# Kernel tuning notes

Measured on AMD Instinct MI355X. Metric: run time of the kernel, lower is better.

Reference implementation:

```python
import jax, jax.numpy as jnp
import numpy as np

B, S, E, H = 4, 1024, 1024, 16
HD = E // H


def setup_inputs() -> dict:
    key = jax.random.key(0)
    k1, k2, k3 = jax.random.split(key, 3)
    hidden_states = jax.random.normal(k1, (B, S, E), dtype=jnp.float32)
    attention_mask = jnp.ones((B, S), dtype=jnp.int32)
    STD = 0.02
    W_qkv = jax.random.normal(k2, (E, 3 * E), dtype=jnp.float32) * STD
    b_qkv = jnp.zeros((3 * E,), dtype=jnp.float32)
    W_proj = jax.random.normal(k3, (E, E), dtype=jnp.float32) * STD
    b_proj = jnp.zeros((E,), dtype=jnp.float32)
    return {
        "hidden_states": hidden_states,
        "attention_mask": attention_mask,
        "W_qkv": W_qkv,
        "b_qkv": b_qkv,
        "W_proj": W_proj,
        "b_proj": b_proj,
    }


def reference(hidden_states, attention_mask, W_qkv, b_qkv, W_proj, b_proj):
    b, s, _ = hidden_states.shape
    dtype = hidden_states.dtype
    qkv = hidden_states @ W_qkv + b_qkv  # [b, s, 3E]
    q, k, v = jnp.split(qkv, 3, axis=-1)

    def split_heads(x):
        return x.reshape(b, s, H, HD).transpose(0, 2, 1, 3)  # [b, H, s, hd]

    q, k, v = split_heads(q), split_heads(k), split_heads(v)
    scale = jnp.asarray(HD, dtype=dtype) ** (-0.5)
    scores = jnp.einsum("bnth,bnsh->bnts", q, k) * scale  # [b, H, s, s]
    causal = jnp.tril(jnp.ones((s, s), dtype=bool))
    key_mask = attention_mask.astype(bool)  # [b, s]
    full_mask = causal[None, None, :, :] & key_mask[:, None, None, :]
    neg = jnp.asarray(jnp.finfo(dtype).min, dtype=dtype)
    bias = jnp.where(full_mask, jnp.asarray(0.0, dtype=dtype), neg)
    probs = jax.nn.softmax(scores + bias, axis=-1)
    out = jnp.einsum("bnts,bnsh->bnth", probs, v)  # [b, H, s, hd]
    out = out.transpose(0, 2, 1, 3).reshape(b, s, E)
    return out @ W_proj + b_proj
```

## Files before the change

### kernel.cpp

```cpp
#include <hip/hip_runtime.h>
#include <stdint.h>

typedef __attribute__((ext_vector_type(8))) short bf16x8;
typedef __attribute__((ext_vector_type(4))) float f32x4;
typedef unsigned short u16;

__device__ __forceinline__ float bf2f(u16 b) {
    unsigned int u = ((unsigned int)b) << 16;
    return __builtin_bit_cast(float, u);
}
__device__ __forceinline__ u16 f2bf(float f) {
    unsigned int u = __builtin_bit_cast(unsigned int, f);
    u += 0x7fffu + ((u >> 16) & 1u);
    return (u16)(u >> 16);
}
__device__ __forceinline__ u16 f2bf_trunc(float f) {
    return (u16)(__builtin_bit_cast(unsigned int, f) >> 16);
}

__device__ __forceinline__ void gl2lds16(const u16* g, u16* l) {
    __builtin_amdgcn_global_load_lds(
        (const __attribute__((address_space(1))) unsigned int*)g,
        (__attribute__((address_space(3))) unsigned int*)l, 16, 0, 0);
}

__global__ __launch_bounds__(256) void cvt_kernel(const float* __restrict__ in,
                                                  u16* __restrict__ out, long n) {
    long i = ((long)blockIdx.x * 256 + threadIdx.x) * 4;
    if (i >= n) return;
    float4 v = *(const float4*)(in + i);
    alignas(8) u16 o[4] = {f2bf(v.x), f2bf(v.y), f2bf(v.z), f2bf(v.w)};
    *(uint2*)(out + i) = *(const uint2*)o;
}

__global__ __launch_bounds__(256) void cvt_transpose(const float* __restrict__ in,
                                                     u16* __restrict__ out, int R, int C) {
    __shared__ float t[64][68];
    int c0 = blockIdx.x * 64, r0 = blockIdx.y * 64, tid = threadIdx.x;
#pragma unroll
    for (int i = 0; i < 4; i++) {
        int ch = i * 256 + tid;
        int r = ch >> 4, cc = (ch & 15) * 4;
        float4 v = *(const float4*)(in + (long)(r0 + r) * C + c0 + cc);
        *(float4*)&t[r][cc] = v;
    }
    __syncthreads();
#pragma unroll
    for (int i = 0; i < 2; i++) {
        int ch = i * 256 + tid;
        int cw = ch >> 3, rr = (ch & 7) * 8;
        alignas(16) u16 tmp[8];
#pragma unroll
        for (int j = 0; j < 8; j++) tmp[j] = f2bf(t[rr + j][cw]);
        *(int4*)(out + (long)(c0 + cw) * R + r0 + rr) = *(const int4*)tmp;
    }
}

__global__ __launch_bounds__(256) void build_vt(const u16* __restrict__ v_tmp,
                                                const int* __restrict__ amask,
                                                u16* __restrict__ vt) {
    __shared__ u16 t[64][72];
    __shared__ u16 mv[64];
    int bh = blockIdx.y, b = bh >> 4, s0 = blockIdx.x * 64, tid = threadIdx.x;
    const u16* inb = v_tmp + ((long)bh * 1024 + s0) * 64;
#pragma unroll
    for (int i = 0; i < 2; i++) {
        int ch = i * 256 + tid;
        int r = ch >> 3, c = (ch & 7) * 8;
        *(int4*)&t[r][c] = *(const int4*)(inb + r * 64 + c);
    }
    if (tid < 64) mv[tid] = amask[b * 1024 + s0 + tid] ? 1 : 0;
    __syncthreads();
    u16* outb = vt + (long)bh * 80 * 1024 + s0;
#pragma unroll
    for (int i = 0; i < 3; i++) {
        int ch = i * 256 + tid;
        if (ch < 640) {
            int row = ch >> 3, c8 = (ch & 7) * 8;
            alignas(16) u16 tmp[8];
#pragma unroll
            for (int jj = 0; jj < 8; jj++) {
                int key = c8 + jj;
                u16 val = (row < 64) ? t[key][row] : ((row == 64) ? (u16)0x3F80 : (u16)0);
                tmp[jj] = mv[key] ? val : (u16)0;
            }
            *(int4*)(outb + (long)row * 1024 + c8) = *(const int4*)tmp;
        }
    }
}

__global__ __launch_bounds__(256) void gemm_bt(
    const u16* __restrict__ X, const u16* __restrict__ Wt,
    const float* __restrict__ bias,
    u16* __restrict__ o0, u16* __restrict__ o1, u16* __restrict__ o2,
    float* __restrict__ outF,
    int M, int N, int K, int mode) {
    __shared__ u16 As[128 * 32];
    __shared__ u16 Bs[128 * 32];
    const int tid = threadIdx.x;
    const int m0 = blockIdx.y * 128, n0 = blockIdx.x * 128;
    const int w = tid >> 6, lane = tid & 63, l16 = lane & 15, quad = lane >> 4;
    const int wm = (w >> 1) * 64, wn = (w & 1) * 64;

    f32x4 acc[4][4];
    const f32x4 z = {0.f, 0.f, 0.f, 0.f};
#pragma unroll
    for (int i = 0; i < 4; i++)
#pragma unroll
        for (int j = 0; j < 4; j++) acc[i][j] = z;

    for (int k0 = 0; k0 < K; k0 += 32) {
        if (k0) __syncthreads();
#pragma unroll
        for (int i = 0; i < 2; i++) {
            int slot = i * 256 + tid;
            int row = slot >> 2, gp = slot & 3;
            int g = gp ^ ((row >> 1) & 3);
            gl2lds16(X + (long)(m0 + row) * K + k0 + g * 8, &As[slot * 8]);
            gl2lds16(Wt + (long)(n0 + row) * K + k0 + g * 8, &Bs[slot * 8]);
        }
        __syncthreads();
        bf16x8 af[4], bfr[4];
#pragma unroll
        for (int mt = 0; mt < 4; mt++) {
            int row = wm + mt * 16 + l16;
            int g = quad ^ ((row >> 1) & 3);
            af[mt] = *(const bf16x8*)&As[row * 32 + g * 8];
        }
#pragma unroll
        for (int nt = 0; nt < 4; nt++) {
            int row = wn + nt * 16 + l16;
            int g = quad ^ ((row >> 1) & 3);
            bfr[nt] = *(const bf16x8*)&Bs[row * 32 + g * 8];
        }
#pragma unroll
        for (int mt = 0; mt < 4; mt++)
#pragma unroll
            for (int nt = 0; nt < 4; nt++)
                acc[mt][nt] = __builtin_amdgcn_mfma_f32_16x16x32_bf16(
                    af[mt], bfr[nt], acc[mt][nt], 0, 0, 0);
    }

#pragma unroll
    for (int nt = 0; nt < 4; nt++) {
        int n = n0 + wn + nt * 16 + l16;
        float bias_v = bias[n];
#pragma unroll
        for (int mt = 0; mt < 4; mt++) {
#pragma unroll
            for (int r = 0; r < 4; r++) {
                int m = m0 + wm + mt * 16 + quad * 4 + r;
                float val = acc[mt][nt][r] + bias_v;
                if (mode == 0) {
                    outF[(long)m * N + n] = val;
                } else {
                    int which = n >> 10, e = n & 1023, h = e >> 6, d = e & 63;
                    int b = m >> 10, s = m & 1023;
                    long adr = ((long)(b * 16 + h) * 1024 + s) * 64 + d;
                    u16* dst = (which == 0) ? o0 : (which == 1) ? o1 : o2;
                    dst[adr] = f2bf(val);
                }
            }
        }
    }
}

#define PPAD 88
__global__ __launch_bounds__(256) void attn_kernel(
    const u16* __restrict__ Q, const u16* __restrict__ K,
    const u16* __restrict__ Vt, u16* __restrict__ O) {
    const int S = 1024;
    const int idx = blockIdx.x;
    const int qb = 15 - (idx >> 6);
    const int bh = idx & 63, b = bh >> 4, h = bh & 15;
    const int tid = threadIdx.x, w = tid >> 6, lane = tid & 63;
    const int l16 = lane & 15, quad = lane >> 4;
    const int q0 = qb * 64 + w * 16;

    __shared__ u16 kt[2][64 * 64];
    __shared__ u16 vt[2][80 * 64];
    __shared__ u16 p_lds[4][16][PPAD];

    const u16* Qb = Q + (long)bh * S * 64;
    const u16* Kb = K + (long)bh * S * 64;
    const u16* Vb = Vt + (long)bh * 80 * S;

    const float C = 0.125f * 1.4426950408889634f;
    bf16x8 qf[2];
#pragma unroll
    for (int kc = 0; kc < 2; kc++) {
        bf16x8 qr = *(const bf16x8*)(Qb + (q0 + l16) * 64 + kc * 32 + quad * 8);
        bf16x8 qs;
#pragma unroll
        for (int e = 0; e < 8; e++) qs[e] = (short)f2bf(bf2f((u16)qr[e]) * C);
        qf[kc] = qs;
    }

    const f32x4 z = {0.f, 0.f, 0.f, 0.f};
    f32x4 o_acc[5];
#pragma unroll
    for (int nt = 0; nt < 5; nt++) o_acc[nt] = z;

    auto prefetch = [&](int j, int pb) {
#pragma unroll
        for (int i = 0; i < 2; i++) {
            int slot = i * 256 + tid;
            int row = slot >> 3, gp = slot & 7;
            int g = gp ^ (row & 7);
            gl2lds16(Kb + (j * 64 + row) * 64 + g * 8, &kt[pb][slot * 8]);
        }
#pragma unroll
        for (int i = 0; i < 3; i++) {
            int slot = i * 256 + tid;
            if (slot < 640) {
                int row = slot >> 3, gp = slot & 7;
                int g = gp ^ (row & 7);
                gl2lds16(Vb + (long)row * S + j * 64 + g * 8, &vt[pb][slot * 8]);
            }
        }
    };

    prefetch(0, 0);
    for (int j = 0; j <= qb; j++) {
        int buf = j & 1;
        __syncthreads();
        if (j < qb) prefetch(j + 1, buf ^ 1);

        f32x4 s_acc[4];
#pragma unroll
        for (int nt = 0; nt < 4; nt++) s_acc[nt] = z;
#pragma unroll
        for (int nt = 0; nt < 4; nt++) {
            int row = nt * 16 + l16;
#pragma unroll
            for (int kc = 0; kc < 2; kc++) {
                int g = (kc * 4 + quad) ^ (row & 7);
                bf16x8 kf = *(const bf16x8*)&kt[buf][row * 64 + g * 8];
                s_acc[nt] = __builtin_amdgcn_mfma_f32_16x16x32_bf16(qf[kc], kf, s_acc[nt], 0, 0, 0);
            }
        }
        float p[4][4];
#pragma unroll
        for (int nt = 0; nt < 4; nt++)
#pragma unroll
            for (int r = 0; r < 4; r++) p[nt][r] = exp2f(s_acc[nt][r]);
        if (j == qb) {
#pragma unroll
            for (int nt = 0; nt < 4; nt++) {
                int key = j * 64 + nt * 16 + l16;
#pragma unroll
                for (int r = 0; r < 4; r++)
                    if (key > q0 + quad * 4 + r) p[nt][r] = 0.f;
            }
        }
#pragma unroll
        for (int nt = 0; nt < 4; nt++)
#pragma unroll
            for (int r = 0; r < 4; r++)
                p_lds[w][quad * 4 + r][nt * 16 + l16] = f2bf_trunc(p[nt][r]);
        bf16x8 pf[2];
#pragma unroll
        for (int kc = 0; kc < 2; kc++)
            pf[kc] = *(const bf16x8*)&p_lds[w][l16][kc * 32 + quad * 8];
#pragma unroll
        for (int nt = 0; nt < 5; nt++) {
            int row = nt * 16 + l16;
#pragma unroll
            for (int kc = 0; kc < 2; kc++) {
                int g = (kc * 4 + quad) ^ (row & 7);
                bf16x8 vf = *(const bf16x8*)&vt[buf][row * 64 + g * 8];
                o_acc[nt] = __builtin_amdgcn_mfma_f32_16x16x32_bf16(pf[kc], vf, o_acc[nt], 0, 0, 0);
            }
        }
    }
#pragma unroll
    for (int r = 0; r < 4; r++) {
        float l = __shfl(o_acc[4][r], lane & 48, 64);
        float inv = 1.0f / l;
        int qg = q0 + quad * 4 + r;
#pragma unroll
        for (int nt = 0; nt < 4; nt++)
            O[((long)(b * S + qg)) * 1024 + h * 64 + nt * 16 + l16] = f2bf(o_acc[nt][r] * inv);
    }
}

extern "C" void kernel_launch(void* const* d_in, const int* in_sizes, int n_in,
                              void* d_out, int out_size, void* d_ws, size_t ws_size,
                              hipStream_t stream) {
    const float* hs    = (const float*)d_in[0];
    const int*   amask = (const int*)d_in[1];
    const float* Wqkv  = (const float*)d_in[2];
    const float* bqkv  = (const float*)d_in[3];
    const float* Wproj = (const float*)d_in[4];
    const float* bproj = (const float*)d_in[5];
    float* out = (float*)d_out;

    const long ME = 4096L * 1024L;
    size_t need = (3072L * 1024 + ME + 1024L * 1024 + 3 * ME) * 2;
    if (ws_size < need) return;

    u16* wqkv_t  = (u16*)d_ws;
    u16* hs_bf   = wqkv_t + 3072L * 1024;
    u16* wproj_t = hs_bf + ME;
    u16* q_ws    = wproj_t + 1024L * 1024;
    u16* k_ws    = q_ws + ME;
    u16* v_tmp   = k_ws + ME;
    u16* vt_aug  = (u16*)d_ws;
    u16* attn_out= v_tmp;

    dim3 blk(256);
    cvt_kernel<<<dim3(4096), blk, 0, stream>>>(hs, hs_bf, ME);
    cvt_transpose<<<dim3(48, 16), blk, 0, stream>>>(Wqkv, wqkv_t, 1024, 3072);
    cvt_transpose<<<dim3(16, 16), blk, 0, stream>>>(Wproj, wproj_t, 1024, 1024);
    gemm_bt<<<dim3(24, 32), blk, 0, stream>>>(hs_bf, wqkv_t, bqkv, q_ws, k_ws, v_tmp,
                                              nullptr, 4096, 3072, 1024, 1);
    build_vt<<<dim3(16, 64), blk, 0, stream>>>(v_tmp, amask, vt_aug);
    attn_kernel<<<dim3(1024), blk, 0, stream>>>(q_ws, k_ws, vt_aug, attn_out);
    gemm_bt<<<dim3(8, 32), blk, 0, stream>>>(attn_out, wproj_t, bproj, nullptr, nullptr, nullptr,
                                             out, 4096, 1024, 1024, 0);
}
```

Measured before the change: 181.9 us.

## Stage QKV GEMM epilogue through LDS and double attention query tile

The QKV GEMM epilogue now converts results to bf16 and stages them in shared memory in two halves, then writes 16-byte vectors to the head-split Q/K/V buffers. Before, each thread wrote scattered 2-byte stores. The attention kernel now handles 128 query rows per block, 32 per wave, so each K/V tile loaded into LDS serves twice as many queries, and the grid is halved to 512 blocks. The costs are an extra 16KB of LDS and more registers in the GEMM, fewer and longer attention blocks with more load imbalance from the causal mask, and waves that sit idle on tiles above their diagonal.

Measured after the change: 201.0 us. 10.5% more time.

```diff
diff --git a/kernel.cpp b/kernel.cpp
--- a/kernel.cpp
+++ b/kernel.cpp
@@ -97,6 +97,7 @@
     int M, int N, int K, int mode) {
     __shared__ u16 As[128 * 32];
     __shared__ u16 Bs[128 * 32];
+    __shared__ u16 ostage[64 * 128];
     const int tid = threadIdx.x;
     const int m0 = blockIdx.y * 128, n0 = blockIdx.x * 128;
     const int w = tid >> 6, lane = tid & 63, l16 = lane & 15, quad = lane >> 4;
@@ -141,65 +142,96 @@
                     af[mt], bfr[nt], acc[mt][nt], 0, 0, 0);
     }
 
-#pragma unroll
-    for (int nt = 0; nt < 4; nt++) {
-        int n = n0 + wn + nt * 16 + l16;
-        float bias_v = bias[n];
-#pragma unroll
-        for (int mt = 0; mt < 4; mt++) {
-#pragma unroll
-            for (int r = 0; r < 4; r++) {
-                int m = m0 + wm + mt * 16 + quad * 4 + r;
-                float val = acc[mt][nt][r] + bias_v;
-                if (mode == 0) {
-                    outF[(long)m * N + n] = val;
-                } else {
-                    int which = n >> 10, e = n & 1023, h = e >> 6, d = e & 63;
-                    int b = m >> 10, s = m & 1023;
-                    long adr = ((long)(b * 16 + h) * 1024 + s) * 64 + d;
-                    u16* dst = (which == 0) ? o0 : (which == 1) ? o1 : o2;
-                    dst[adr] = f2bf(val);
+    if (mode == 0) {
+#pragma unroll
+        for (int nt = 0; nt < 4; nt++) {
+            int n = n0 + wn + nt * 16 + l16;
+            float bias_v = bias[n];
+#pragma unroll
+            for (int mt = 0; mt < 4; mt++)
+#pragma unroll
+                for (int r = 0; r < 4; r++) {
+                    int m = m0 + wm + mt * 16 + quad * 4 + r;
+                    outF[(long)m * N + n] = acc[mt][nt][r] + bias_v;
                 }
-            }
-        }
-    }
-}
-
-#define PPAD 88
+        }
+    } else {
+#pragma unroll
+        for (int p = 0; p < 2; p++) {
+            if (p) __syncthreads();
+            if ((w >> 1) == p) {
+#pragma unroll
+                for (int nt = 0; nt < 4; nt++) {
+                    int col = wn + nt * 16 + l16;
+                    float bias_v = bias[n0 + col];
+#pragma unroll
+                    for (int mt = 0; mt < 4; mt++)
+#pragma unroll
+                        for (int r = 0; r < 4; r++) {
+                            int row = mt * 16 + quad * 4 + r;
+                            int gs = (col >> 3) ^ ((row >> 1) & 7);
+                            ostage[row * 128 + gs * 8 + (col & 7)] =
+                                f2bf(acc[mt][nt][r] + bias_v);
+                        }
+                }
+            }
+            __syncthreads();
+#pragma unroll
+            for (int i = 0; i < 4; i++) {
+                int g = i * 256 + tid;
+                int rr = g >> 4, c = (g >> 3) & 1, seg = g & 7;
+                int gs = (c * 8 + seg) ^ ((rr >> 1) & 7);
+                int4 v = *(const int4*)&ostage[rr * 128 + gs * 8];
+                int m = m0 + p * 64 + rr;
+                int nbase = n0 + c * 64;
+                int which = nbase >> 10, e = nbase & 1023, hh = e >> 6;
+                int bb = m >> 10, s = m & 1023;
+                u16* dst = (which == 0) ? o0 : (which == 1) ? o1 : o2;
+                *(int4*)(dst + (((long)(bb * 16 + hh) * 1024 + s) * 64 + seg * 8)) = v;
+            }
+        }
+    }
+}
+
+#define QPAD 76
 __global__ __launch_bounds__(256) void attn_kernel(
     const u16* __restrict__ Q, const u16* __restrict__ K,
     const u16* __restrict__ Vt, u16* __restrict__ O) {
     const int S = 1024;
     const int idx = blockIdx.x;
-    const int qb = 15 - (idx >> 6);
+    const int qb = 7 - (idx >> 6);
     const int bh = idx & 63, b = bh >> 4, h = bh & 15;
     const int tid = threadIdx.x, w = tid >> 6, lane = tid & 63;
     const int l16 = lane & 15, quad = lane >> 4;
-    const int q0 = qb * 64 + w * 16;
+    const int q0 = qb * 128 + w * 32;
 
     __shared__ u16 kt[2][64 * 64];
     __shared__ u16 vt[2][80 * 64];
-    __shared__ u16 p_lds[4][16][PPAD];
+    __shared__ u16 p_lds[4][32][QPAD];
 
     const u16* Qb = Q + (long)bh * S * 64;
     const u16* Kb = K + (long)bh * S * 64;
     const u16* Vb = Vt + (long)bh * 80 * S;
 
     const float C = 0.125f * 1.4426950408889634f;
-    bf16x8 qf[2];
-#pragma unroll
-    for (int kc = 0; kc < 2; kc++) {
-        bf16x8 qr = *(const bf16x8*)(Qb + (q0 + l16) * 64 + kc * 32 + quad * 8);
-        bf16x8 qs;
-#pragma unroll
-        for (int e = 0; e < 8; e++) qs[e] = (short)f2bf(bf2f((u16)qr[e]) * C);
-        qf[kc] = qs;
-    }
+    bf16x8 qf[2][2];
+#pragma unroll
+    for (int qt = 0; qt < 2; qt++)
+#pragma unroll
+        for (int kc = 0; kc < 2; kc++) {
+            bf16x8 qr = *(const bf16x8*)(Qb + (q0 + qt * 16 + l16) * 64 + kc * 32 + quad * 8);
+            bf16x8 qs;
+#pragma unroll
+            for (int e = 0; e < 8; e++) qs[e] = (short)f2bf(bf2f((u16)qr[e]) * C);
+            qf[qt][kc] = qs;
+        }
 
     const f32x4 z = {0.f, 0.f, 0.f, 0.f};
-    f32x4 o_acc[5];
-#pragma unroll
-    for (int nt = 0; nt < 5; nt++) o_acc[nt] = z;
+    f32x4 o_acc[2][5];
+#pragma unroll
+    for (int qt = 0; qt < 2; qt++)
+#pragma unroll
+        for (int nt = 0; nt < 5; nt++) o_acc[qt][nt] = z;
 
     auto prefetch = [&](int j, int pb) {
 #pragma unroll
@@ -221,67 +253,90 @@
     };
 
     prefetch(0, 0);
-    for (int j = 0; j <= qb; j++) {
+    const int jmax = 2 * qb + 1;
+    for (int j = 0; j <= jmax; j++) {
         int buf = j & 1;
         __syncthreads();
-        if (j < qb) prefetch(j + 1, buf ^ 1);
-
-        f32x4 s_acc[4];
-#pragma unroll
-        for (int nt = 0; nt < 4; nt++) s_acc[nt] = z;
-#pragma unroll
-        for (int nt = 0; nt < 4; nt++) {
-            int row = nt * 16 + l16;
-#pragma unroll
-            for (int kc = 0; kc < 2; kc++) {
-                int g = (kc * 4 + quad) ^ (row & 7);
-                bf16x8 kf = *(const bf16x8*)&kt[buf][row * 64 + g * 8];
-                s_acc[nt] = __builtin_amdgcn_mfma_f32_16x16x32_bf16(qf[kc], kf, s_acc[nt], 0, 0, 0);
-            }
-        }
-        float p[4][4];
-#pragma unroll
-        for (int nt = 0; nt < 4; nt++)
-#pragma unroll
-            for (int r = 0; r < 4; r++) p[nt][r] = exp2f(s_acc[nt][r]);
-        if (j == qb) {
+        if (j < jmax) prefetch(j + 1, buf ^ 1);
+
+        if (j * 64 <= q0 + 31) {
+            f32x4 s_acc[2][4];
+#pragma unroll
+            for (int qt = 0; qt < 2; qt++)
+#pragma unroll
+                for (int nt = 0; nt < 4; nt++) s_acc[qt][nt] = z;
 #pragma unroll
             for (int nt = 0; nt < 4; nt++) {
-                int key = j * 64 + nt * 16 + l16;
-#pragma unroll
-                for (int r = 0; r < 4; r++)
-                    if (key > q0 + quad * 4 + r) p[nt][r] = 0.f;
-            }
-        }
-#pragma unroll
-        for (int nt = 0; nt < 4; nt++)
-#pragma unroll
-            for (int r = 0; r < 4; r++)
-                p_lds[w][quad * 4 + r][nt * 16 + l16] = f2bf_trunc(p[nt][r]);
-        bf16x8 pf[2];
-#pragma unroll
-        for (int kc = 0; kc < 2; kc++)
-            pf[kc] = *(const bf16x8*)&p_lds[w][l16][kc * 32 + quad * 8];
-#pragma unroll
-        for (int nt = 0; nt < 5; nt++) {
-            int row = nt * 16 + l16;
-#pragma unroll
-            for (int kc = 0; kc < 2; kc++) {
-                int g = (kc * 4 + quad) ^ (row & 7);
-                bf16x8 vf = *(const bf16x8*)&vt[buf][row * 64 + g * 8];
-                o_acc[nt] = __builtin_amdgcn_mfma_f32_16x16x32_bf16(pf[kc], vf, o_acc[nt], 0, 0, 0);
-            }
-        }
-    }
-#pragma unroll
-    for (int r = 0; r < 4; r++) {
-        float l = __shfl(o_acc[4][r], lane & 48, 64);
-        float inv = 1.0f / l;
-        int qg = q0 + quad * 4 + r;
-#pragma unroll
-        for (int nt = 0; nt < 4; nt++)
-            O[((long)(b * S + qg)) * 1024 + h * 64 + nt * 16 + l16] = f2bf(o_acc[nt][r] * inv);
-    }
+                int row = nt * 16 + l16;
+#pragma unroll
+                for (int kc = 0; kc < 2; kc++) {
+                    int g = (kc * 4 + quad) ^ (row & 7);
+                    bf16x8 kf = *(const bf16x8*)&kt[buf][row * 64 + g * 8];
+#pragma unroll
+                    for (int qt = 0; qt < 2; qt++)
+                        s_acc[qt][nt] = __builtin_amdgcn_mfma_f32_16x16x32_bf16(
+                            qf[qt][kc], kf, s_acc[qt][nt], 0, 0, 0);
+                }
+            }
+            float p[2][4][4];
+#pragma unroll
+            for (int qt = 0; qt < 2; qt++)
+#pragma unroll
+                for (int nt = 0; nt < 4; nt++)
+#pragma unroll
+                    for (int r = 0; r < 4; r++) p[qt][nt][r] = exp2f(s_acc[qt][nt][r]);
+            if (j * 64 + 63 > q0) {
+#pragma unroll
+                for (int qt = 0; qt < 2; qt++)
+#pragma unroll
+                    for (int nt = 0; nt < 4; nt++) {
+                        int key = j * 64 + nt * 16 + l16;
+#pragma unroll
+                        for (int r = 0; r < 4; r++)
+                            if (key > q0 + qt * 16 + quad * 4 + r) p[qt][nt][r] = 0.f;
+                    }
+            }
+#pragma unroll
+            for (int qt = 0; qt < 2; qt++)
+#pragma unroll
+                for (int nt = 0; nt < 4; nt++)
+#pragma unroll
+                    for (int r = 0; r < 4; r++)
+                        p_lds[w][qt * 16 + quad * 4 + r][nt * 16 + l16] =
+                            f2bf_trunc(p[qt][nt][r]);
+            bf16x8 pf[2][2];
+#pragma unroll
+            for (int qt = 0; qt < 2; qt++)
+#pragma unroll
+                for (int kc = 0; kc < 2; kc++)
+                    pf[qt][kc] = *(const bf16x8*)&p_lds[w][qt * 16 + l16][kc * 32 + quad * 8];
+#pragma unroll
+            for (int vtile = 0; vtile < 5; vtile++) {
+                int row = vtile * 16 + l16;
+#pragma unroll
+                for (int kc = 0; kc < 2; kc++) {
+                    int g = (kc * 4 + quad) ^ (row & 7);
+                    bf16x8 vf = *(const bf16x8*)&vt[buf][row * 64 + g * 8];
+#pragma unroll
+                    for (int qt = 0; qt < 2; qt++)
+                        o_acc[qt][vtile] = __builtin_amdgcn_mfma_f32_16x16x32_bf16(
+                            pf[qt][kc], vf, o_acc[qt][vtile], 0, 0, 0);
+                }
+            }
+        }
+    }
+#pragma unroll
+    for (int qt = 0; qt < 2; qt++)
+#pragma unroll
+        for (int r = 0; r < 4; r++) {
+            float l = __shfl(o_acc[qt][4][r], lane & 48, 64);
+            float inv = 1.0f / l;
+            int qg = q0 + qt * 16 + quad * 4 + r;
+#pragma unroll
+            for (int nt = 0; nt < 4; nt++)
+                O[((long)(b * S + qg)) * 1024 + h * 64 + nt * 16 + l16] =
+                    f2bf(o_acc[qt][nt][r] * inv);
+        }
 }
 
 extern "C" void kernel_launch(void* const* d_in, const int* in_sizes, int n_in,
@@ -315,7 +370,7 @@
     gemm_bt<<<dim3(24, 32), blk, 0, stream>>>(hs_bf, wqkv_t, bqkv, q_ws, k_ws, v_tmp,
                                               nullptr, 4096, 3072, 1024, 1);
     build_vt<<<dim3(16, 64), blk, 0, stream>>>(v_tmp, amask, vt_aug);
-    attn_kernel<<<dim3(1024), blk, 0, stream>>>(q_ws, k_ws, vt_aug, attn_out);
+    attn_kernel<<<dim3(512), blk, 0, stream>>>(q_ws, k_ws, vt_aug, attn_out);
     gemm_bt<<<dim3(8, 32), blk, 0, stream>>>(attn_out, wproj_t, bproj, nullptr, nullptr, nullptr,
                                              out, 4096, 1024, 1024, 0);
 }
```

## Stage QKV GEMM epilogue through LDS for vectorized head-layout stores

Applied to the files above, without the earlier changes.

The GEMM warp tiling changes from a 2x2 arrangement of 64x64 tiles to four warps that each cover all 128 rows and a 32-column strip, so every warp reads all A fragments and two B fragments. In QKV mode the bf16 results are written into swizzled shared memory in two halves and then stored to the per-head Q/K/V layout as 16-byte vector writes. This replaces scattered 2-byte stores. It adds extra barriers and LDS traffic, and gives a different A/B fragment-load balance.

Result: slower. 192.5 us (+5.8%).

```diff
diff --git a/kernel.cpp b/kernel.cpp
--- a/kernel.cpp
+++ b/kernel.cpp
@@ -95,19 +95,20 @@
     u16* __restrict__ o0, u16* __restrict__ o1, u16* __restrict__ o2,
     float* __restrict__ outF,
     int M, int N, int K, int mode) {
-    __shared__ u16 As[128 * 32];
-    __shared__ u16 Bs[128 * 32];
+    __shared__ u16 smem[8192];
+    u16* As = smem;
+    u16* Bs = smem + 4096;
     const int tid = threadIdx.x;
     const int m0 = blockIdx.y * 128, n0 = blockIdx.x * 128;
     const int w = tid >> 6, lane = tid & 63, l16 = lane & 15, quad = lane >> 4;
-    const int wm = (w >> 1) * 64, wn = (w & 1) * 64;
-
-    f32x4 acc[4][4];
+    const int wn = w * 32;
+
+    f32x4 acc[8][2];
     const f32x4 z = {0.f, 0.f, 0.f, 0.f};
 #pragma unroll
-    for (int i = 0; i < 4; i++)
-#pragma unroll
-        for (int j = 0; j < 4; j++) acc[i][j] = z;
+    for (int i = 0; i < 8; i++)
+#pragma unroll
+        for (int j = 0; j < 2; j++) acc[i][j] = z;
 
     for (int k0 = 0; k0 < K; k0 += 32) {
         if (k0) __syncthreads();
@@ -120,46 +121,75 @@
             gl2lds16(Wt + (long)(n0 + row) * K + k0 + g * 8, &Bs[slot * 8]);
         }
         __syncthreads();
-        bf16x8 af[4], bfr[4];
-#pragma unroll
-        for (int mt = 0; mt < 4; mt++) {
-            int row = wm + mt * 16 + l16;
+        bf16x8 af[8], bfr[2];
+#pragma unroll
+        for (int mt = 0; mt < 8; mt++) {
+            int row = mt * 16 + l16;
             int g = quad ^ ((row >> 1) & 3);
             af[mt] = *(const bf16x8*)&As[row * 32 + g * 8];
         }
 #pragma unroll
-        for (int nt = 0; nt < 4; nt++) {
+        for (int nt = 0; nt < 2; nt++) {
             int row = wn + nt * 16 + l16;
             int g = quad ^ ((row >> 1) & 3);
             bfr[nt] = *(const bf16x8*)&Bs[row * 32 + g * 8];
         }
 #pragma unroll
-        for (int mt = 0; mt < 4; mt++)
-#pragma unroll
-            for (int nt = 0; nt < 4; nt++)
+        for (int mt = 0; mt < 8; mt++)
+#pragma unroll
+            for (int nt = 0; nt < 2; nt++)
                 acc[mt][nt] = __builtin_amdgcn_mfma_f32_16x16x32_bf16(
                     af[mt], bfr[nt], acc[mt][nt], 0, 0, 0);
     }
 
-#pragma unroll
-    for (int nt = 0; nt < 4; nt++) {
-        int n = n0 + wn + nt * 16 + l16;
-        float bias_v = bias[n];
-#pragma unroll
-        for (int mt = 0; mt < 4; mt++) {
-#pragma unroll
-            for (int r = 0; r < 4; r++) {
-                int m = m0 + wm + mt * 16 + quad * 4 + r;
-                float val = acc[mt][nt][r] + bias_v;
-                if (mode == 0) {
-                    outF[(long)m * N + n] = val;
-                } else {
-                    int which = n >> 10, e = n & 1023, h = e >> 6, d = e & 63;
-                    int b = m >> 10, s = m & 1023;
-                    long adr = ((long)(b * 16 + h) * 1024 + s) * 64 + d;
-                    u16* dst = (which == 0) ? o0 : (which == 1) ? o1 : o2;
-                    dst[adr] = f2bf(val);
+    if (mode == 0) {
+#pragma unroll
+        for (int nt = 0; nt < 2; nt++) {
+            int n = n0 + wn + nt * 16 + l16;
+            float bias_v = bias[n];
+#pragma unroll
+            for (int mt = 0; mt < 8; mt++)
+#pragma unroll
+                for (int r = 0; r < 4; r++) {
+                    int m = m0 + mt * 16 + quad * 4 + r;
+                    outF[(long)m * N + n] = acc[mt][nt][r] + bias_v;
                 }
+        }
+    } else {
+        __syncthreads();
+        u16* ostage = smem;
+#pragma unroll
+        for (int p = 0; p < 2; p++) {
+            if (p) __syncthreads();
+#pragma unroll
+            for (int mt = 0; mt < 4; mt++) {
+                int mtg = p * 4 + mt;
+#pragma unroll
+                for (int nt = 0; nt < 2; nt++) {
+                    int col = wn + nt * 16 + l16;
+                    float bias_v = bias[n0 + col];
+#pragma unroll
+                    for (int r = 0; r < 4; r++) {
+                        int row = mt * 16 + quad * 4 + r;
+                        int gs = (col >> 3) ^ ((row >> 1) & 7);
+                        ostage[row * 128 + gs * 8 + (col & 7)] =
+                            f2bf(acc[mtg][nt][r] + bias_v);
+                    }
+                }
+            }
+            __syncthreads();
+#pragma unroll
+            for (int i = 0; i < 4; i++) {
+                int g = i * 256 + tid;
+                int rr = g >> 4, c = (g >> 3) & 1, seg = g & 7;
+                int gs = (c * 8 + seg) ^ ((rr >> 1) & 7);
+                int4 v = *(const int4*)&ostage[rr * 128 + gs * 8];
+                int m = m0 + p * 64 + rr;
+                int nbase = n0 + c * 64;
+                int which = nbase >> 10, e = nbase & 1023, hh = e >> 6;
+                int bb = m >> 10, s = m & 1023;
+                u16* dst = (which == 0) ? o0 : (which == 1) ? o1 : o2;
+                *(int4*)(dst + (((long)(bb * 16 + hh) * 1024 + s) * 64 + seg * 8)) = v;
             }
         }
     }
```

## Fuse prep kernels, write masked transposed V from QKV GEMM, retile projection

Applied to the files above, without the earlier changes.

Merges the three conversion/transpose kernels into one launch. The QKV GEMM epilogue now writes V directly in transposed, masked form with a ones-row for the softmax denominator, which removes the separate build_vt pass and its round trip through memory. The attention kernel now loads only 65 V rows instead of 80 and zero-fills the padding rows in LDS once. The output projection moves to a dedicated 128x64-tile kernel with twice as many blocks. The trade-off is strided 2-byte scattered stores for transposed V in the GEMM epilogue, plus an extra mask-row load in each prefetch.

Result: faster. 174.9 us (-3.9%).

```diff
diff --git a/kernel.cpp b/kernel.cpp
--- a/kernel.cpp
+++ b/kernel.cpp
@@ -24,19 +24,31 @@
         (__attribute__((address_space(3))) unsigned int*)l, 16, 0, 0);
 }
 
-__global__ __launch_bounds__(256) void cvt_kernel(const float* __restrict__ in,
-                                                  u16* __restrict__ out, long n) {
-    long i = ((long)blockIdx.x * 256 + threadIdx.x) * 4;
-    if (i >= n) return;
-    float4 v = *(const float4*)(in + i);
-    alignas(8) u16 o[4] = {f2bf(v.x), f2bf(v.y), f2bf(v.z), f2bf(v.w)};
-    *(uint2*)(out + i) = *(const uint2*)o;
-}
-
-__global__ __launch_bounds__(256) void cvt_transpose(const float* __restrict__ in,
-                                                     u16* __restrict__ out, int R, int C) {
+__global__ __launch_bounds__(256) void prep_kernel(
+    const float* __restrict__ hs, const float* __restrict__ Wqkv,
+    const float* __restrict__ Wproj, u16* __restrict__ hs_bf,
+    u16* __restrict__ wqkv_t, u16* __restrict__ wproj_t) {
     __shared__ float t[64][68];
-    int c0 = blockIdx.x * 64, r0 = blockIdx.y * 64, tid = threadIdx.x;
+    int bx = blockIdx.x, tid = threadIdx.x;
+    if (bx < 4096) {
+        long i = ((long)bx * 256 + tid) * 4;
+        float4 v = *(const float4*)(hs + i);
+        alignas(8) u16 o[4] = {f2bf(v.x), f2bf(v.y), f2bf(v.z), f2bf(v.w)};
+        *(uint2*)(hs_bf + i) = *(const uint2*)o;
+        return;
+    }
+    const float* in;
+    u16* out;
+    int R = 1024, C, c0, r0;
+    if (bx < 4864) {
+        int tt = bx - 4096;
+        C = 3072; c0 = (tt % 48) * 64; r0 = (tt / 48) * 64;
+        in = Wqkv; out = wqkv_t;
+    } else {
+        int tt = bx - 4864;
+        C = 1024; c0 = (tt % 16) * 64; r0 = (tt / 16) * 64;
+        in = Wproj; out = wproj_t;
+    }
 #pragma unroll
     for (int i = 0; i < 4; i++) {
         int ch = i * 256 + tid;
@@ -56,45 +68,11 @@
     }
 }
 
-__global__ __launch_bounds__(256) void build_vt(const u16* __restrict__ v_tmp,
-                                                const int* __restrict__ amask,
-                                                u16* __restrict__ vt) {
-    __shared__ u16 t[64][72];
-    __shared__ u16 mv[64];
-    int bh = blockIdx.y, b = bh >> 4, s0 = blockIdx.x * 64, tid = threadIdx.x;
-    const u16* inb = v_tmp + ((long)bh * 1024 + s0) * 64;
-#pragma unroll
-    for (int i = 0; i < 2; i++) {
-        int ch = i * 256 + tid;
-        int r = ch >> 3, c = (ch & 7) * 8;
-        *(int4*)&t[r][c] = *(const int4*)(inb + r * 64 + c);
-    }
-    if (tid < 64) mv[tid] = amask[b * 1024 + s0 + tid] ? 1 : 0;
-    __syncthreads();
-    u16* outb = vt + (long)bh * 80 * 1024 + s0;
-#pragma unroll
-    for (int i = 0; i < 3; i++) {
-        int ch = i * 256 + tid;
-        if (ch < 640) {
-            int row = ch >> 3, c8 = (ch & 7) * 8;
-            alignas(16) u16 tmp[8];
-#pragma unroll
-            for (int jj = 0; jj < 8; jj++) {
-                int key = c8 + jj;
-                u16 val = (row < 64) ? t[key][row] : ((row == 64) ? (u16)0x3F80 : (u16)0);
-                tmp[jj] = mv[key] ? val : (u16)0;
-            }
-            *(int4*)(outb + (long)row * 1024 + c8) = *(const int4*)tmp;
-        }
-    }
-}
-
-__global__ __launch_bounds__(256) void gemm_bt(
+__global__ __launch_bounds__(256) void gemm_qkv(
     const u16* __restrict__ X, const u16* __restrict__ Wt,
-    const float* __restrict__ bias,
-    u16* __restrict__ o0, u16* __restrict__ o1, u16* __restrict__ o2,
-    float* __restrict__ outF,
-    int M, int N, int K, int mode) {
+    const float* __restrict__ bias, const int* __restrict__ amask,
+    u16* __restrict__ q_ws, u16* __restrict__ k_ws, u16* __restrict__ vt_ws,
+    int K) {
     __shared__ u16 As[128 * 32];
     __shared__ u16 Bs[128 * 32];
     const int tid = threadIdx.x;
@@ -141,27 +119,40 @@
                     af[mt], bfr[nt], acc[mt][nt], 0, 0, 0);
     }
 
+    const int which = n0 >> 10;
+    const int b = m0 >> 10;
+    int ncol[4]; float bv[4];
 #pragma unroll
     for (int nt = 0; nt < 4; nt++) {
-        int n = n0 + wn + nt * 16 + l16;
-        float bias_v = bias[n];
-#pragma unroll
-        for (int mt = 0; mt < 4; mt++) {
-#pragma unroll
-            for (int r = 0; r < 4; r++) {
-                int m = m0 + wm + mt * 16 + quad * 4 + r;
-                float val = acc[mt][nt][r] + bias_v;
-                if (mode == 0) {
-                    outF[(long)m * N + n] = val;
-                } else {
-                    int which = n >> 10, e = n & 1023, h = e >> 6, d = e & 63;
-                    int b = m >> 10, s = m & 1023;
-                    long adr = ((long)(b * 16 + h) * 1024 + s) * 64 + d;
-                    u16* dst = (which == 0) ? o0 : (which == 1) ? o1 : o2;
-                    dst[adr] = f2bf(val);
-                }
-            }
-        }
+        ncol[nt] = n0 + wn + nt * 16 + l16;
+        bv[nt] = bias[ncol[nt]];
+    }
+#pragma unroll
+    for (int mt = 0; mt < 4; mt++) {
+#pragma unroll
+        for (int r = 0; r < 4; r++) {
+            int m = m0 + wm + mt * 16 + quad * 4 + r;
+            int s = m & 1023;
+            float mk = 1.f;
+            if (which == 2) mk = amask[b * 1024 + s] ? 1.f : 0.f;
+#pragma unroll
+            for (int nt = 0; nt < 4; nt++) {
+                int e = ncol[nt] & 1023, h = e >> 6, d = e & 63;
+                float val = acc[mt][nt][r] + bv[nt];
+                if (which == 0)
+                    q_ws[((long)(b * 16 + h) * 1024 + s) * 64 + d] = f2bf(val);
+                else if (which == 1)
+                    k_ws[((long)(b * 16 + h) * 1024 + s) * 64 + d] = f2bf(val);
+                else
+                    vt_ws[((long)(b * 16 + h) * 65 + d) * 1024 + s] = f2bf(val * mk);
+            }
+        }
+    }
+    if (which == 2) {
+        int hh = ((n0 & 1023) >> 6) + (tid >> 7);
+        int s = (m0 & 1023) + (tid & 127);
+        vt_ws[((long)(b * 16 + hh) * 65 + 64) * 1024 + s] =
+            amask[b * 1024 + s] ? (u16)0x3F80 : (u16)0;
     }
 }
 
@@ -183,7 +174,14 @@
 
     const u16* Qb = Q + (long)bh * S * 64;
     const u16* Kb = K + (long)bh * S * 64;
-    const u16* Vb = Vt + (long)bh * 80 * S;
+    const u16* Vb = Vt + (long)bh * 65 * S;
+
+    if (tid < 240) {
+        int bufi = tid >= 120, rem = tid - bufi * 120;
+        int row = 65 + (rem >> 3), gp = rem & 7;
+        const int4 z4 = {0, 0, 0, 0};
+        *(int4*)&vt[bufi][row * 64 + gp * 8] = z4;
+    }
 
     const float C = 0.125f * 1.4426950408889634f;
     bf16x8 qf[2];
@@ -202,6 +200,9 @@
     for (int nt = 0; nt < 5; nt++) o_acc[nt] = z;
 
     auto prefetch = [&](int j, int pb) {
+        int4 mrow;
+        if (tid < 8)
+            mrow = *(const int4*)(Vb + 64 * S + j * 64 + tid * 8);
 #pragma unroll
         for (int i = 0; i < 2; i++) {
             int slot = i * 256 + tid;
@@ -210,14 +211,14 @@
             gl2lds16(Kb + (j * 64 + row) * 64 + g * 8, &kt[pb][slot * 8]);
         }
 #pragma unroll
-        for (int i = 0; i < 3; i++) {
+        for (int i = 0; i < 2; i++) {
             int slot = i * 256 + tid;
-            if (slot < 640) {
-                int row = slot >> 3, gp = slot & 7;
-                int g = gp ^ (row & 7);
-                gl2lds16(Vb + (long)row * S + j * 64 + g * 8, &vt[pb][slot * 8]);
-            }
-        }
+            int row = slot >> 3, gp = slot & 7;
+            int g = gp ^ (row & 7);
+            gl2lds16(Vb + (long)row * S + j * 64 + g * 8, &vt[pb][slot * 8]);
+        }
+        if (tid < 8)
+            *(int4*)&vt[pb][64 * 64 + tid * 8] = mrow;
     };
 
     prefetch(0, 0);
@@ -281,6 +282,74 @@
 #pragma unroll
         for (int nt = 0; nt < 4; nt++)
             O[((long)(b * S + qg)) * 1024 + h * 64 + nt * 16 + l16] = f2bf(o_acc[nt][r] * inv);
+    }
+}
+
+__global__ __launch_bounds__(256) void gemm_proj(
+    const u16* __restrict__ X, const u16* __restrict__ Wt,
+    const float* __restrict__ bias, float* __restrict__ outF, int K) {
+    __shared__ u16 As[128 * 32];
+    __shared__ u16 Bs[64 * 32];
+    const int tid = threadIdx.x;
+    const int m0 = blockIdx.y * 128, n0 = blockIdx.x * 64;
+    const int w = tid >> 6, lane = tid & 63, l16 = lane & 15, quad = lane >> 4;
+    const int wm = (w >> 1) * 64, wn = (w & 1) * 32;
+    const int N = 1024;
+
+    f32x4 acc[4][2];
+    const f32x4 z = {0.f, 0.f, 0.f, 0.f};
+#pragma unroll
+    for (int i = 0; i < 4; i++)
+#pragma unroll
+        for (int j = 0; j < 2; j++) acc[i][j] = z;
+
+    for (int k0 = 0; k0 < K; k0 += 32) {
+        if (k0) __syncthreads();
+#pragma unroll
+        for (int i = 0; i < 2; i++) {
+            int slot = i * 256 + tid;
+            int row = slot >> 2, gp = slot & 3;
+            int g = gp ^ ((row >> 1) & 3);
+            gl2lds16(X + (long)(m0 + row) * K + k0 + g * 8, &As[slot * 8]);
+        }
+        {
+            int slot = tid;
+            int row = slot >> 2, gp = slot & 3;
+            int g = gp ^ ((row >> 1) & 3);
+            gl2lds16(Wt + (long)(n0 + row) * K + k0 + g * 8, &Bs[slot * 8]);
+        }
+        __syncthreads();
+        bf16x8 af[4], bfr[2];
+#pragma unroll
+        for (int mt = 0; mt < 4; mt++) {
+            int row = wm + mt * 16 + l16;
+            int g = quad ^ ((row >> 1) & 3);
+            af[mt] = *(const bf16x8*)&As[row * 32 + g * 8];
+        }
+#pragma unroll
+        for (int nt = 0; nt < 2; nt++) {
+            int row = wn + nt * 16 + l16;
+            int g = quad ^ ((row >> 1) & 3);
+            bfr[nt] = *(const bf16x8*)&Bs[row * 32 + g * 8];
+        }
+#pragma unroll
+        for (int mt = 0; mt < 4; mt++)
+#pragma unroll
+            for (int nt = 0; nt < 2; nt++)
+                acc[mt][nt] = __builtin_amdgcn_mfma_f32_16x16x32_bf16(
+                    af[mt], bfr[nt], acc[mt][nt], 0, 0, 0);
+    }
+#pragma unroll
+    for (int nt = 0; nt < 2; nt++) {
+        int n = n0 + wn + nt * 16 + l16;
+        float bias_v = bias[n];
+#pragma unroll
+        for (int mt = 0; mt < 4; mt++)
+#pragma unroll
+            for (int r = 0; r < 4; r++) {
+                int m = m0 + wm + mt * 16 + quad * 4 + r;
+                outF[(long)m * N + n] = acc[mt][nt][r] + bias_v;
+            }
     }
 }
 
@@ -296,7 +365,8 @@
     float* out = (float*)d_out;
 
     const long ME = 4096L * 1024L;
-    size_t need = (3072L * 1024 + ME + 1024L * 1024 + 3 * ME) * 2;
+    const long VT = 65L * 1024L * 64L;
+    size_t need = (3072L * 1024 + ME + 1024L * 1024 + 2 * ME + VT) * 2;
     if (ws_size < need) return;
 
     u16* wqkv_t  = (u16*)d_ws;
@@ -304,18 +374,13 @@
     u16* wproj_t = hs_bf + ME;
     u16* q_ws    = wproj_t + 1024L * 1024;
     u16* k_ws    = q_ws + ME;
-    u16* v_tmp   = k_ws + ME;
-    u16* vt_aug  = (u16*)d_ws;
-    u16* attn_out= v_tmp;
+    u16* vt_ws   = k_ws + ME;
+    u16* attn_out= (u16*)d_ws;
 
     dim3 blk(256);
-    cvt_kernel<<<dim3(4096), blk, 0, stream>>>(hs, hs_bf, ME);
-    cvt_transpose<<<dim3(48, 16), blk, 0, stream>>>(Wqkv, wqkv_t, 1024, 3072);
-    cvt_transpose<<<dim3(16, 16), blk, 0, stream>>>(Wproj, wproj_t, 1024, 1024);
-    gemm_bt<<<dim3(24, 32), blk, 0, stream>>>(hs_bf, wqkv_t, bqkv, q_ws, k_ws, v_tmp,
-                                              nullptr, 4096, 3072, 1024, 1);
-    build_vt<<<dim3(16, 64), blk, 0, stream>>>(v_tmp, amask, vt_aug);
-    attn_kernel<<<dim3(1024), blk, 0, stream>>>(q_ws, k_ws, vt_aug, attn_out);
-    gemm_bt<<<dim3(8, 32), blk, 0, stream>>>(attn_out, wproj_t, bproj, nullptr, nullptr, nullptr,
-                                             out, 4096, 1024, 1024, 0);
-}
+    prep_kernel<<<dim3(5120), blk, 0, stream>>>(hs, Wqkv, Wproj, hs_bf, wqkv_t, wproj_t);
+    gemm_qkv<<<dim3(24, 32), blk, 0, stream>>>(hs_bf, wqkv_t, bqkv, amask,
+                                               q_ws, k_ws, vt_ws, 1024);
+    attn_kernel<<<dim3(1024), blk, 0, stream>>>(q_ws, k_ws, vt_ws, attn_out);
+    gemm_proj<<<dim3(16, 32), blk, 0, stream>>>(attn_out, wproj_t, bproj, out, 1024);
+}
```
